# Kernel tuning notes

Hardware: AMD Instinct MI355X
Metric: run time of the kernel (lower is better)

The kernel has to match this reference:

```python
import jax, jax.numpy as jnp
import numpy as np

DIM = 128
HEADS = 8
HEAD_DIM = DIM // HEADS
K = 5          # kernel_size per spatial axis
DIL = 1        # dilation
EPS = 1e-5


def setup_inputs() -> dict:
    key = jax.random.key(0)
    ks = jax.random.split(key, 12)
    s = 0.02
    inp = {
        "x": jax.random.normal(ks[0], (1, DIM, 16, 16, 4), jnp.float32),
        "skip": jax.random.normal(ks[1], (1, DIM, 32, 32, 8), jnp.float32),
        "Wq": jax.random.normal(ks[2], (DIM, DIM), jnp.float32) * s,
        "bq": jnp.zeros((DIM,), jnp.float32),
        "Wk": jax.random.normal(ks[3], (DIM, DIM), jnp.float32) * s,
        "bk": jnp.zeros((DIM,), jnp.float32),
        "Wv": jax.random.normal(ks[4], (DIM, DIM), jnp.float32) * s,
        "bv": jnp.zeros((DIM,), jnp.float32),
        "rpb": jax.random.normal(ks[5], (HEADS, 2 * K - 1, 2 * K - 1, 2 * K - 1), jnp.float32) * s,
        "Wo": jax.random.normal(ks[6], (DIM, DIM), jnp.float32) * s,
        "bo": jnp.zeros((DIM,), jnp.float32),
    }
    return inp


def _instance_norm(t):
    # InstanceNorm3d, affine=False: normalize over spatial dims per (B, C)
    mu = jnp.mean(t, axis=(2, 3, 4), keepdims=True)
    var = jnp.var(t, axis=(2, 3, 4), keepdims=True)
    return (t - mu) * jax.lax.rsqrt(var + EPS)


def _nbr_idx(L):
    # NATTEN-style clamped window: start shifted to stay in bounds
    i = np.arange(L)
    start = np.clip(i - (K // 2) * DIL, 0, L - 1 - (K - 1) * DIL)
    idx = start[:, None] + np.arange(K)[None, :] * DIL  # (L, K)
    rel = (idx - i[:, None]) // DIL + (K - 1)           # (L, K) in [0, 2K-2]
    return jnp.asarray(idx), jnp.asarray(rel)


def reference(x, skip, Wq, bq, Wk, bk, Wv, bv, rpb, Wo, bo):
    x = _instance_norm(x)
    skip = _instance_norm(skip)

    xu = jnp.repeat(jnp.repeat(jnp.repeat(x, 2, axis=2), 2, axis=3), 2, axis=4)

    B, C, H, W, Z = skip.shape
    N = H * W * Z
    xt = xu.transpose(0, 2, 3, 4, 1).reshape(B, N, C)    # queries from upsampled x
    st = skip.transpose(0, 2, 3, 4, 1).reshape(B, N, C)  # keys/values from skip

    def heads(t):
        return t.reshape(B, N, HEADS, HEAD_DIM).transpose(0, 2, 1, 3)  # (B,h,N,d)

    q = heads(xt @ Wq + bq) * (HEAD_DIM ** -0.5)
    k = heads(st @ Wk + bk)
    v = heads(st @ Wv + bv)

    idxH, relH = _nbr_idx(H)
    idxW, relW = _nbr_idx(W)
    idxZ, relZ = _nbr_idx(Z)

    # flattened neighbor token indices: (N, K^3)
    nbr = (idxH[:, None, None, :, None, None] * (W * Z)
           + idxW[None, :, None, None, :, None] * Z
           + idxZ[None, None, :, None, None, :])
    nbr = jnp.broadcast_to(nbr, (H, W, Z, K, K, K)).reshape(N, K ** 3)

    # relative position bias gather: (heads, N, K^3)
    rH = jnp.broadcast_to(relH[:, None, None, :, None, None], (H, W, Z, K, K, K)).reshape(N, K ** 3)
    rW = jnp.broadcast_to(relW[None, :, None, None, :, None], (H, W, Z, K, K, K)).reshape(N, K ** 3)
    rZ = jnp.broadcast_to(relZ[None, None, :, None, None, :], (H, W, Z, K, K, K)).reshape(N, K ** 3)
    bias = rpb[:, rH, rW, rZ]  # (heads, N, K^3)

    kg = jnp.take(k, nbr, axis=2)  # (B, h, N, K^3, d)
    vg = jnp.take(v, nbr, axis=2)

    logits = jnp.einsum('bhnd,bhnkd->bhnk', q, kg) + bias[None]
    attn = jax.nn.softmax(logits, axis=-1)
    out = jnp.einsum('bhnk,bhnkd->bhnd', attn, vg)

    out = out.transpose(0, 2, 1, 3).reshape(B, N, C) @ Wo + bo
    return out.reshape(B, H, W, Z, C).transpose(0, 4, 1, 2, 3)
```

## Files before the change

kernel.cpp:

```cpp
#include <hip/hip_runtime.h>
#include <math.h>

#define DIM 128
#define HEADS 8
#define HD 16
#define NPOS 8192
#define EPS 1e-5f

typedef _Float16 half2_t __attribute__((ext_vector_type(2)));

static __device__ __forceinline__ half2_t u2h(unsigned u) {
    half2_t r; __builtin_memcpy(&r, &u, 4); return r;
}
static __device__ __forceinline__ unsigned pkh(float a, float b) {
    half2_t h; h.x = (_Float16)a; h.y = (_Float16)b;
    unsigned u; __builtin_memcpy(&u, &h, 4); return u;
}
static __device__ __forceinline__ float dot2(unsigned k, unsigned q, float acc) {
#if __has_builtin(__builtin_amdgcn_fdot2)
    return __builtin_amdgcn_fdot2(u2h(k), u2h(q), acc, false);
#else
    half2_t kh = u2h(k), qh = u2h(q);
    acc = fmaf((float)kh.x, (float)qh.x, acc);
    return fmaf((float)kh.y, (float)qh.y, acc);
#endif
}

__global__ __launch_bounds__(256) void stats_kernel(const float* __restrict__ x,
                                                    const float* __restrict__ skip,
                                                    float* __restrict__ ws) {
    int c = blockIdx.x;
    const float* src; int n; float* mu_out; float* rs_out; int ci;
    if (c < DIM) { ci = c; src = x + c * 1024; n = 1024; mu_out = ws; rs_out = ws + DIM; }
    else { ci = c - DIM; src = skip + (size_t)ci * NPOS; n = NPOS; mu_out = ws + 2*DIM; rs_out = ws + 3*DIM; }
    int t = threadIdx.x;
    const float4* s4 = (const float4*)src;
    int n4 = n >> 2;
    float s = 0.f, s2 = 0.f;
    for (int i = t; i < n4; i += 256) {
        float4 v = s4[i];
        s += (v.x + v.y) + (v.z + v.w);
        s2 = fmaf(v.x, v.x, fmaf(v.y, v.y, fmaf(v.z, v.z, fmaf(v.w, v.w, s2))));
    }
    #pragma unroll
    for (int off = 32; off > 0; off >>= 1) {
        s  += __shfl_down(s,  off, 64);
        s2 += __shfl_down(s2, off, 64);
    }
    __shared__ float ls[4], ls2[4];
    int wv = t >> 6;
    if ((t & 63) == 0) { ls[wv] = s; ls2[wv] = s2; }
    __syncthreads();
    if (t == 0) {
        float S  = ls[0] + ls[1] + ls[2] + ls[3];
        float S2 = ls2[0] + ls2[1] + ls2[2] + ls2[3];
        float inv_n = 1.f / (float)n;
        float mu  = S * inv_n;
        float var = S2 * inv_n - mu * mu;
        mu_out[ci] = mu;
        rs_out[ci] = rsqrtf(var + EPS);
    }
}

__global__ __launch_bounds__(256) void qkv_kernel(const float* __restrict__ x,
                                                  const float* __restrict__ skip,
                                                  const float* __restrict__ Wq, const float* __restrict__ bq,
                                                  const float* __restrict__ Wk, const float* __restrict__ bk,
                                                  const float* __restrict__ Wv, const float* __restrict__ bv,
                                                  const float* __restrict__ ws,
                                                  unsigned* __restrict__ q_out,
                                                  unsigned* __restrict__ k_out,
                                                  unsigned* __restrict__ v_out) {
    __shared__ float at[128 * 68];
    __shared__ float wl[128 * 64];
    int which = blockIdx.y;
    if (which == 0 && blockIdx.x >= 16) return;
    int t = threadIdx.x;
    int half  = blockIdx.z;
    int n0 = blockIdx.x * 64;

    const float* W = (which == 0) ? Wq : (which == 1) ? Wk : Wv;
    const float* b = (which == 0) ? bq : (which == 1) ? bk : bv;
    {
        const float4* W4 = (const float4*)W;
        float4* wl4 = (float4*)wl;
        for (int i4 = t; i4 < 2048; i4 += 256) {
            int ci = i4 >> 4, j4 = i4 & 15;
            wl4[ci * 16 + j4] = W4[ci * 32 + half * 16 + j4];
        }
    }
    const float* mu = (which == 0) ? ws : ws + 2*DIM;
    const float* rs = (which == 0) ? ws + DIM : ws + 3*DIM;
    if (which == 0) {
        for (int i4 = t; i4 < 2048; i4 += 256) {
            int ci = i4 >> 4, ln4 = (i4 & 15) * 4;
            float4 f = *(const float4*)(x + ci * 1024 + n0 + ln4);
            float m_ = mu[ci], r_ = rs[ci];
            *(float4*)(at + ci * 68 + ln4) =
                make_float4((f.x - m_) * r_, (f.y - m_) * r_, (f.z - m_) * r_, (f.w - m_) * r_);
        }
    } else {
        for (int i4 = t; i4 < 2048; i4 += 256) {
            int ci = i4 >> 4, ln4 = (i4 & 15) * 4;
            float4 f = *(const float4*)(skip + (size_t)ci * NPOS + n0 + ln4);
            float m_ = mu[ci], r_ = rs[ci];
            *(float4*)(at + ci * 68 + ln4) =
                make_float4((f.x - m_) * r_, (f.y - m_) * r_, (f.z - m_) * r_, (f.w - m_) * r_);
        }
    }
    __syncthreads();

    int pg = t & 15, cg = t >> 4;
    float4 bv4 = *(const float4*)(b + half * 64 + cg * 4);
    float4 acc[4];
    #pragma unroll
    for (int ps = 0; ps < 4; ++ps) acc[ps] = bv4;

    const float* ap = at + pg * 4;
    const float* wp = wl + cg * 4;
    #pragma unroll 4
    for (int ci = 0; ci < 128; ++ci) {
        float4 a4 = *(const float4*)(ap + ci * 68);
        float4 w4 = *(const float4*)(wp + ci * 64);
        float av[4] = { a4.x, a4.y, a4.z, a4.w };
        #pragma unroll
        for (int ps = 0; ps < 4; ++ps) {
            float a = av[ps];
            acc[ps].x = fmaf(a, w4.x, acc[ps].x);
            acc[ps].y = fmaf(a, w4.y, acc[ps].y);
            acc[ps].z = fmaf(a, w4.z, acc[ps].z);
            acc[ps].w = fmaf(a, w4.w, acc[ps].w);
        }
    }
    int p0 = n0 + pg * 4;
    if (which == 0) {
        #pragma unroll
        for (int ps = 0; ps < 4; ++ps) {
            uint2 pk;
            pk.x = pkh(acc[ps].x * 0.25f, acc[ps].y * 0.25f);
            pk.y = pkh(acc[ps].z * 0.25f, acc[ps].w * 0.25f);
            *(uint2*)(q_out + (size_t)(p0 + ps) * 64 + half * 32 + cg * 2) = pk;
        }
    } else {
        unsigned* outp = (which == 1) ? k_out : v_out;
        #pragma unroll
        for (int ps = 0; ps < 4; ++ps) {
            uint2 pk;
            pk.x = pkh(acc[ps].x, acc[ps].y);
            pk.y = pkh(acc[ps].z, acc[ps].w);
            *(uint2*)(outp + (size_t)(p0 + ps) * 64 + half * 32 + cg * 2) = pk;
        }
    }
}

__global__ __launch_bounds__(512, 4) void attn_kernel(const unsigned* __restrict__ qb,
                                                      const unsigned* __restrict__ kb,
                                                      const unsigned* __restrict__ vb,
                                                      const float* __restrict__ rpb,
                                                      float* __restrict__ ao_t) {
    __shared__ uint4 kbf[2 * 544];
    __shared__ uint4 vbf[2 * 544];
    __shared__ float bias_l[744];

    int blk = blockIdx.x;
    int h    = blk & 7;
    int tile = blk >> 3;
    int h0 = (tile >> 3) * 4;
    int w0 = (tile & 7) * 4;
    int bh0 = min(max(h0 - 2, 0), 24);
    int bw0 = min(max(w0 - 2, 0), 24);
    int t = threadIdx.x;

    for (int idx = t; idx < 1024; idx += 512) {
        int c2 = idx & 1;
        int r  = idx >> 1;
        int gz = r & 7;
        int q2 = r >> 3;
        int gh = q2 >> 3, gw = q2 & 7;
        int n = (bh0 + gh) * 256 + (bw0 + gw) * 8 + gz;
        int base = gh * 68 + gw * 8 + ((gz + gw) & 7);
        kbf[c2 * 544 + base] = *(const uint4*)(kb + (size_t)n * 64 + h * 8 + c2 * 4);
        vbf[c2 * 544 + base] = *(const uint4*)(vb + (size_t)n * 64 + h * 8 + c2 * 4);
    }
    for (int idx = t; idx < 744; idx += 512) bias_l[idx] = (idx < 729) ? rpb[h * 729 + idx] : 0.f;
    __syncthreads();

    int s = t & 7, p = t >> 3;
    int ph = p >> 4, pw = (p >> 2) & 3, pzp = p & 3;
    int hc = h0 + ph, wc = w0 + pw, zc0 = pzp * 2;
    int sh = min(max(hc - 2, 0), 27);
    int sw = min(max(wc - 2, 0), 27);
    int sz0 = min(max(zc0 - 2, 0), 3);
    int sz1 = min(max(zc0 - 1, 0), 3);
    int dlt = sz1 - sz0;
    int hb = sh - bh0, wb = sw - bw0;
    int b0 = (sh - hc + 4) * 81 + (sw - wc + 4) * 9 + (sz0 - zc0 + 4);
    int n0pos = hc * 256 + wc * 8 + zc0;

    int qrow = (hc >> 1) * 64 + (wc >> 1) * 4 + pzp;
    uint4 qa = *(const uint4*)(qb + (size_t)qrow * 64 + h * 8);
    uint4 qc = *(const uint4*)(qb + (size_t)qrow * 64 + h * 8 + 4);

    float o0[16], o1[16];
    #pragma unroll
    for (int d = 0; d < 16; ++d) { o0[d] = 0.f; o1[d] = 0.f; }
    float l0 = 0.f, l1 = 0.f;

    int cnt   = 18 + (s < 6);
    int start = s * 18 + min(s, 6);
    int i0 = p & 15;

    for (int it = 0; it < cnt; ++it) {
        int ii = i0 + it; if (ii >= cnt) ii -= cnt;
        int j = start + ii;
        int jh = (j * 2185) >> 16;
        int jr = j - jh * 30;
        int jw = (jr * 43) >> 8;
        int jz = jr - jw * 6;
        int gw = wb + jw;
        int gz = sz0 + jz;
        int base = (hb + jh) * 68 + gw * 8 + ((gz + gw) & 7);
        int joff = jh * 81 + jw * 9 + jz;
        float bias1 = bias_l[b0 + joff - 1];
        float bias0 = bias_l[b0 + joff];

        uint4 ka = kbf[base];
        uint4 k2 = kbf[544 + base];
        float d0 = dot2(ka.x, qa.x, 0.f);
        float d1 = dot2(ka.y, qa.y, 0.f);
        d0 = dot2(ka.z, qa.z, d0);
        d1 = dot2(ka.w, qa.w, d1);
        d0 = dot2(k2.x, qc.x, d0);
        d1 = dot2(k2.y, qc.y, d1);
        d0 = dot2(k2.z, qc.z, d0);
        d1 = dot2(k2.w, qc.w, d1);
        float d = d0 + d1;

        bool v0ok = (jz < 5);
        bool v1ok = ((unsigned)(jz - dlt) < 5u);
        float e0 = __expf(d + bias0);
        float e1 = __expf(d + bias1);
        float pp0 = v0ok ? e0 : 0.f;
        float pp1 = v1ok ? e1 : 0.f;
        l0 += pp0; l1 += pp1;

        uint4 va = vbf[base];
        uint4 v2 = vbf[544 + base];
        #define PV(u, dd) { half2_t vh = u2h(u); float f0 = (float)vh.x, f1 = (float)vh.y; \
            o0[dd]   = fmaf(pp0, f0, o0[dd]);   o1[dd]   = fmaf(pp1, f0, o1[dd]); \
            o0[dd+1] = fmaf(pp0, f1, o0[dd+1]); o1[dd+1] = fmaf(pp1, f1, o1[dd+1]); }
        PV(va.x, 0)  PV(va.y, 2)  PV(va.z, 4)  PV(va.w, 6)
        PV(v2.x, 8)  PV(v2.y, 10) PV(v2.z, 12) PV(v2.w, 14)
        #undef PV
    }

    #pragma unroll
    for (int step = 1; step <= 4; step <<= 1) {
        l0 += __shfl_xor(l0, step, 64);
        l1 += __shfl_xor(l1, step, 64);
        #pragma unroll
        for (int d = 0; d < 16; ++d) {
            o0[d] += __shfl_xor(o0[d], step, 64);
            o1[d] += __shfl_xor(o1[d], step, 64);
        }
    }
    float inv0 = 1.f / l0, inv1 = 1.f / l1;
    int row = h * 16 + 2 * s;
    float2 r0 = make_float2(o0[2*s]     * inv0, o1[2*s]     * inv1);
    float2 r1 = make_float2(o0[2*s + 1] * inv0, o1[2*s + 1] * inv1);
    *(float2*)(ao_t + (size_t)row       * NPOS + n0pos) = r0;
    *(float2*)(ao_t + (size_t)(row + 1) * NPOS + n0pos) = r1;
}

__global__ __launch_bounds__(256) void proj_kernel(const float* __restrict__ ao_t,
                                                   const float* __restrict__ Wo,
                                                   const float* __restrict__ bo,
                                                   float* __restrict__ out) {
    __shared__ float at[128 * 68];
    __shared__ float wl[128 * 64];
    int t = threadIdx.x;
    int half = blockIdx.y;
    int n0 = blockIdx.x * 64;

    {
        const float4* W4 = (const float4*)Wo;
        float4* wl4 = (float4*)wl;
        for (int i4 = t; i4 < 2048; i4 += 256) {
            int ci = i4 >> 4, j4 = i4 & 15;
            wl4[ci * 16 + j4] = W4[ci * 32 + half * 16 + j4];
        }
    }
    for (int i4 = t; i4 < 2048; i4 += 256) {
        int ci = i4 >> 4, ln4 = (i4 & 15) * 4;
        float4 f = *(const float4*)(ao_t + (size_t)ci * NPOS + n0 + ln4);
        *(float4*)(at + ci * 68 + ln4) = f;
    }
    __syncthreads();

    int pg = t & 15, cg = t >> 4;
    float4 bv4 = *(const float4*)(bo + half * 64 + cg * 4);
    float4 acc[4];
    #pragma unroll
    for (int ps = 0; ps < 4; ++ps) acc[ps] = bv4;

    const float* ap = at + pg * 4;
    const float* wp = wl + cg * 4;
    #pragma unroll 4
    for (int ci = 0; ci < 128; ++ci) {
        float4 a4 = *(const float4*)(ap + ci * 68);
        float4 w4 = *(const float4*)(wp + ci * 64);
        float av[4] = { a4.x, a4.y, a4.z, a4.w };
        #pragma unroll
        for (int ps = 0; ps < 4; ++ps) {
            float a = av[ps];
            acc[ps].x = fmaf(a, w4.x, acc[ps].x);
            acc[ps].y = fmaf(a, w4.y, acc[ps].y);
            acc[ps].z = fmaf(a, w4.z, acc[ps].z);
            acc[ps].w = fmaf(a, w4.w, acc[ps].w);
        }
    }
    int p0 = n0 + pg * 4;
    int jbase = half * 64 + cg * 4;
    *(float4*)(out + (size_t)(jbase + 0) * NPOS + p0) = make_float4(acc[0].x, acc[1].x, acc[2].x, acc[3].x);
    *(float4*)(out + (size_t)(jbase + 1) * NPOS + p0) = make_float4(acc[0].y, acc[1].y, acc[2].y, acc[3].y);
    *(float4*)(out + (size_t)(jbase + 2) * NPOS + p0) = make_float4(acc[0].z, acc[1].z, acc[2].z, acc[3].z);
    *(float4*)(out + (size_t)(jbase + 3) * NPOS + p0) = make_float4(acc[0].w, acc[1].w, acc[2].w, acc[3].w);
}

extern "C" void kernel_launch(void* const* d_in, const int* in_sizes, int n_in,
                              void* d_out, int out_size, void* d_ws, size_t ws_size,
                              hipStream_t stream) {
    const float* x    = (const float*)d_in[0];
    const float* skip = (const float*)d_in[1];
    const float* Wq   = (const float*)d_in[2];
    const float* bq   = (const float*)d_in[3];
    const float* Wk   = (const float*)d_in[4];
    const float* bk   = (const float*)d_in[5];
    const float* Wv   = (const float*)d_in[6];
    const float* bv   = (const float*)d_in[7];
    const float* rpb  = (const float*)d_in[8];
    const float* Wo   = (const float*)d_in[9];
    const float* bo   = (const float*)d_in[10];
    float* out = (float*)d_out;

    float*    ws   = (float*)d_ws;
    unsigned* q    = (unsigned*)(ws + 512);
    unsigned* kbp  = q + 1024 * 64;
    unsigned* vbp  = kbp + (size_t)NPOS * 64;
    float*    ao_t = (float*)(vbp + (size_t)NPOS * 64);

    stats_kernel<<<256, 256, 0, stream>>>(x, skip, ws);
    qkv_kernel<<<dim3(128, 3, 2), 256, 0, stream>>>(x, skip, Wq, bq, Wk, bk, Wv, bv, ws, q, kbp, vbp);
    attn_kernel<<<512, 512, 0, stream>>>(q, kbp, vbp, rpb, ao_t);
    proj_kernel<<<dim3(128, 2), 256, 0, stream>>>(ao_t, Wo, bo, out);
}
```

Before: 129.7 us.

## Use 128x128 fp16-staged tiles with 8x8 register blocking in QKV and projection GEMMs

Both the QKV and output-projection kernels now handle 128 positions by all 128 output channels per block. Activations and weights are staged in shared memory as fp16 to fit the larger tile, and each thread accumulates an 8x8 register block instead of 4x4. This removes the split over output-channel halves, so inputs are loaded once and each shared-memory read feeds more FMAs. In exchange the grids shrink to 64 blocks (fewer than the CU count), register pressure rises, and the projection input ao_t is now rounded to fp16, which adds precision loss.

```diff
diff --git a/kernel.cpp b/kernel.cpp
--- a/kernel.cpp
+++ b/kernel.cpp
@@ -71,84 +71,98 @@
                                                   unsigned* __restrict__ q_out,
                                                   unsigned* __restrict__ k_out,
                                                   unsigned* __restrict__ v_out) {
-    __shared__ float at[128 * 68];
-    __shared__ float wl[128 * 64];
+    __shared__ __align__(16) _Float16 ah[128 * 128];
+    __shared__ __align__(16) _Float16 wh[128 * 128];
     int which = blockIdx.y;
-    if (which == 0 && blockIdx.x >= 16) return;
+    if (which == 0 && blockIdx.x >= 8) return;
     int t = threadIdx.x;
-    int half  = blockIdx.z;
-    int n0 = blockIdx.x * 64;
+    int n0 = blockIdx.x * 128;
 
     const float* W = (which == 0) ? Wq : (which == 1) ? Wk : Wv;
     const float* b = (which == 0) ? bq : (which == 1) ? bk : bv;
+    const float* mu = (which == 0) ? ws : ws + 2*DIM;
+    const float* rs = (which == 0) ? ws + DIM : ws + 3*DIM;
+
     {
         const float4* W4 = (const float4*)W;
-        float4* wl4 = (float4*)wl;
-        for (int i4 = t; i4 < 2048; i4 += 256) {
-            int ci = i4 >> 4, j4 = i4 & 15;
-            wl4[ci * 16 + j4] = W4[ci * 32 + half * 16 + j4];
-        }
-    }
-    const float* mu = (which == 0) ? ws : ws + 2*DIM;
-    const float* rs = (which == 0) ? ws + DIM : ws + 3*DIM;
+        for (int i4 = t; i4 < 4096; i4 += 256) {
+            int ci = i4 >> 5, j4 = i4 & 31;
+            float4 w = W4[ci * 32 + j4];
+            *(uint2*)&wh[ci * 128 + j4 * 4] = make_uint2(pkh(w.x, w.y), pkh(w.z, w.w));
+        }
+    }
     if (which == 0) {
-        for (int i4 = t; i4 < 2048; i4 += 256) {
-            int ci = i4 >> 4, ln4 = (i4 & 15) * 4;
-            float4 f = *(const float4*)(x + ci * 1024 + n0 + ln4);
+        const float4* x4 = (const float4*)x;
+        for (int i4 = t; i4 < 4096; i4 += 256) {
+            int ci = i4 >> 5, j4 = i4 & 31;
+            float4 f = x4[ci * 256 + (n0 >> 2) + j4];
             float m_ = mu[ci], r_ = rs[ci];
-            *(float4*)(at + ci * 68 + ln4) =
-                make_float4((f.x - m_) * r_, (f.y - m_) * r_, (f.z - m_) * r_, (f.w - m_) * r_);
+            *(uint2*)&ah[ci * 128 + j4 * 4] =
+                make_uint2(pkh((f.x - m_) * r_, (f.y - m_) * r_),
+                           pkh((f.z - m_) * r_, (f.w - m_) * r_));
         }
     } else {
-        for (int i4 = t; i4 < 2048; i4 += 256) {
-            int ci = i4 >> 4, ln4 = (i4 & 15) * 4;
-            float4 f = *(const float4*)(skip + (size_t)ci * NPOS + n0 + ln4);
+        for (int i4 = t; i4 < 4096; i4 += 256) {
+            int ci = i4 >> 5, j4 = i4 & 31;
+            float4 f = *(const float4*)(skip + (size_t)ci * NPOS + n0 + j4 * 4);
             float m_ = mu[ci], r_ = rs[ci];
-            *(float4*)(at + ci * 68 + ln4) =
-                make_float4((f.x - m_) * r_, (f.y - m_) * r_, (f.z - m_) * r_, (f.w - m_) * r_);
+            *(uint2*)&ah[ci * 128 + j4 * 4] =
+                make_uint2(pkh((f.x - m_) * r_, (f.y - m_) * r_),
+                           pkh((f.z - m_) * r_, (f.w - m_) * r_));
         }
     }
     __syncthreads();
 
     int pg = t & 15, cg = t >> 4;
-    float4 bv4 = *(const float4*)(b + half * 64 + cg * 4);
-    float4 acc[4];
-    #pragma unroll
-    for (int ps = 0; ps < 4; ++ps) acc[ps] = bv4;
-
-    const float* ap = at + pg * 4;
-    const float* wp = wl + cg * 4;
+    float4 b0 = *(const float4*)(b + cg * 8);
+    float4 b1 = *(const float4*)(b + cg * 8 + 4);
+    float acc[8][8];
+    #pragma unroll
+    for (int p = 0; p < 8; ++p) {
+        acc[p][0] = b0.x; acc[p][1] = b0.y; acc[p][2] = b0.z; acc[p][3] = b0.w;
+        acc[p][4] = b1.x; acc[p][5] = b1.y; acc[p][6] = b1.z; acc[p][7] = b1.w;
+    }
+
+    const _Float16* ap = ah + pg * 8;
+    const _Float16* wp = wh + cg * 8;
     #pragma unroll 4
     for (int ci = 0; ci < 128; ++ci) {
-        float4 a4 = *(const float4*)(ap + ci * 68);
-        float4 w4 = *(const float4*)(wp + ci * 64);
-        float av[4] = { a4.x, a4.y, a4.z, a4.w };
-        #pragma unroll
-        for (int ps = 0; ps < 4; ++ps) {
-            float a = av[ps];
-            acc[ps].x = fmaf(a, w4.x, acc[ps].x);
-            acc[ps].y = fmaf(a, w4.y, acc[ps].y);
-            acc[ps].z = fmaf(a, w4.z, acc[ps].z);
-            acc[ps].w = fmaf(a, w4.w, acc[ps].w);
-        }
-    }
-    int p0 = n0 + pg * 4;
+        uint4 au = *(const uint4*)(ap + ci * 128);
+        uint4 wu = *(const uint4*)(wp + ci * 128);
+        half2_t a0 = u2h(au.x), a1 = u2h(au.y), a2 = u2h(au.z), a3 = u2h(au.w);
+        half2_t w0 = u2h(wu.x), w1 = u2h(wu.y), w2 = u2h(wu.z), w3 = u2h(wu.w);
+        float af[8] = { (float)a0.x, (float)a0.y, (float)a1.x, (float)a1.y,
+                        (float)a2.x, (float)a2.y, (float)a3.x, (float)a3.y };
+        float wf[8] = { (float)w0.x, (float)w0.y, (float)w1.x, (float)w1.y,
+                        (float)w2.x, (float)w2.y, (float)w3.x, (float)w3.y };
+        #pragma unroll
+        for (int p = 0; p < 8; ++p)
+            #pragma unroll
+            for (int c = 0; c < 8; ++c)
+                acc[p][c] = fmaf(af[p], wf[c], acc[p][c]);
+    }
+
+    int p0 = n0 + pg * 8;
     if (which == 0) {
         #pragma unroll
-        for (int ps = 0; ps < 4; ++ps) {
-            uint2 pk;
-            pk.x = pkh(acc[ps].x * 0.25f, acc[ps].y * 0.25f);
-            pk.y = pkh(acc[ps].z * 0.25f, acc[ps].w * 0.25f);
-            *(uint2*)(q_out + (size_t)(p0 + ps) * 64 + half * 32 + cg * 2) = pk;
+        for (int p = 0; p < 8; ++p) {
+            uint4 o;
+            o.x = pkh(acc[p][0] * 0.25f, acc[p][1] * 0.25f);
+            o.y = pkh(acc[p][2] * 0.25f, acc[p][3] * 0.25f);
+            o.z = pkh(acc[p][4] * 0.25f, acc[p][5] * 0.25f);
+            o.w = pkh(acc[p][6] * 0.25f, acc[p][7] * 0.25f);
+            *(uint4*)(q_out + (size_t)(p0 + p) * 64 + cg * 4) = o;
         }
     } else {
         unsigned* outp = (which == 1) ? k_out : v_out;
         #pragma unroll
-        for (int ps = 0; ps < 4; ++ps) {
-            uint2 pk;
-            pk.x = pkh(acc[ps].x, acc[ps].y);
-            pk.y = pkh(acc[ps].z, acc[ps].w);
-            *(uint2*)(outp + (size_t)(p0 + ps) * 64 + half * 32 + cg * 2) = pk;
+        for (int p = 0; p < 8; ++p) {
+            uint4 o;
+            o.x = pkh(acc[p][0], acc[p][1]);
+            o.y = pkh(acc[p][2], acc[p][3]);
+            o.z = pkh(acc[p][4], acc[p][5]);
+            o.w = pkh(acc[p][6], acc[p][7]);
+            *(uint4*)(outp + (size_t)(p0 + p) * 64 + cg * 4) = o;
         }
     }
 }
@@ -276,55 +290,63 @@
                                                    const float* __restrict__ Wo,
                                                    const float* __restrict__ bo,
                                                    float* __restrict__ out) {
-    __shared__ float at[128 * 68];
-    __shared__ float wl[128 * 64];
+    __shared__ __align__(16) _Float16 ah[128 * 128];
+    __shared__ __align__(16) _Float16 wh[128 * 128];
     int t = threadIdx.x;
-    int half = blockIdx.y;
-    int n0 = blockIdx.x * 64;
+    int n0 = blockIdx.x * 128;
 
     {
         const float4* W4 = (const float4*)Wo;
-        float4* wl4 = (float4*)wl;
-        for (int i4 = t; i4 < 2048; i4 += 256) {
-            int ci = i4 >> 4, j4 = i4 & 15;
-            wl4[ci * 16 + j4] = W4[ci * 32 + half * 16 + j4];
-        }
-    }
-    for (int i4 = t; i4 < 2048; i4 += 256) {
-        int ci = i4 >> 4, ln4 = (i4 & 15) * 4;
-        float4 f = *(const float4*)(ao_t + (size_t)ci * NPOS + n0 + ln4);
-        *(float4*)(at + ci * 68 + ln4) = f;
+        for (int i4 = t; i4 < 4096; i4 += 256) {
+            int ci = i4 >> 5, j4 = i4 & 31;
+            float4 w = W4[ci * 32 + j4];
+            *(uint2*)&wh[ci * 128 + j4 * 4] = make_uint2(pkh(w.x, w.y), pkh(w.z, w.w));
+        }
+    }
+    for (int i4 = t; i4 < 4096; i4 += 256) {
+        int ci = i4 >> 5, j4 = i4 & 31;
+        float4 f = *(const float4*)(ao_t + (size_t)ci * NPOS + n0 + j4 * 4);
+        *(uint2*)&ah[ci * 128 + j4 * 4] = make_uint2(pkh(f.x, f.y), pkh(f.z, f.w));
     }
     __syncthreads();
 
     int pg = t & 15, cg = t >> 4;
-    float4 bv4 = *(const float4*)(bo + half * 64 + cg * 4);
-    float4 acc[4];
-    #pragma unroll
-    for (int ps = 0; ps < 4; ++ps) acc[ps] = bv4;
-
-    const float* ap = at + pg * 4;
-    const float* wp = wl + cg * 4;
+    float4 b0 = *(const float4*)(bo + cg * 8);
+    float4 b1 = *(const float4*)(bo + cg * 8 + 4);
+    float acc[8][8];
+    #pragma unroll
+    for (int p = 0; p < 8; ++p) {
+        acc[p][0] = b0.x; acc[p][1] = b0.y; acc[p][2] = b0.z; acc[p][3] = b0.w;
+        acc[p][4] = b1.x; acc[p][5] = b1.y; acc[p][6] = b1.z; acc[p][7] = b1.w;
+    }
+
+    const _Float16* ap = ah + pg * 8;
+    const _Float16* wp = wh + cg * 8;
     #pragma unroll 4
     for (int ci = 0; ci < 128; ++ci) {
-        float4 a4 = *(const float4*)(ap + ci * 68);
-        float4 w4 = *(const float4*)(wp + ci * 64);
-        float av[4] = { a4.x, a4.y, a4.z, a4.w };
-        #pragma unroll
-        for (int ps = 0; ps < 4; ++ps) {
-            float a = av[ps];
-            acc[ps].x = fmaf(a, w4.x, acc[ps].x);
-            acc[ps].y = fmaf(a, w4.y, acc[ps].y);
-            acc[ps].z = fmaf(a, w4.z, acc[ps].z);
-            acc[ps].w = fmaf(a, w4.w, acc[ps].w);
-        }
-    }
-    int p0 = n0 + pg * 4;
-    int jbase = half * 64 + cg * 4;
-    *(float4*)(out + (size_t)(jbase + 0) * NPOS + p0) = make_float4(acc[0].x, acc[1].x, acc[2].x, acc[3].x);
-    *(float4*)(out + (size_t)(jbase + 1) * NPOS + p0) = make_float4(acc[0].y, acc[1].y, acc[2].y, acc[3].y);
-    *(float4*)(out + (size_t)(jbase + 2) * NPOS + p0) = make_float4(acc[0].z, acc[1].z, acc[2].z, acc[3].z);
-    *(float4*)(out + (size_t)(jbase + 3) * NPOS + p0) = make_float4(acc[0].w, acc[1].w, acc[2].w, acc[3].w);
+        uint4 au = *(const uint4*)(ap + ci * 128);
+        uint4 wu = *(const uint4*)(wp + ci * 128);
+        half2_t a0 = u2h(au.x), a1 = u2h(au.y), a2 = u2h(au.z), a3 = u2h(au.w);
+        half2_t w0 = u2h(wu.x), w1 = u2h(wu.y), w2 = u2h(wu.z), w3 = u2h(wu.w);
+        float af[8] = { (float)a0.x, (float)a0.y, (float)a1.x, (float)a1.y,
+                        (float)a2.x, (float)a2.y, (float)a3.x, (float)a3.y };
+        float wf[8] = { (float)w0.x, (float)w0.y, (float)w1.x, (float)w1.y,
+                        (float)w2.x, (float)w2.y, (float)w3.x, (float)w3.y };
+        #pragma unroll
+        for (int p = 0; p < 8; ++p)
+            #pragma unroll
+            for (int c = 0; c < 8; ++c)
+                acc[p][c] = fmaf(af[p], wf[c], acc[p][c]);
+    }
+
+    int p0 = n0 + pg * 8;
+    int co0 = cg * 8;
+    #pragma unroll
+    for (int c = 0; c < 8; ++c) {
+        float* op = out + (size_t)(co0 + c) * NPOS + p0;
+        *(float4*)op       = make_float4(acc[0][c], acc[1][c], acc[2][c], acc[3][c]);
+        *(float4*)(op + 4) = make_float4(acc[4][c], acc[5][c], acc[6][c], acc[7][c]);
+    }
 }
 
 extern "C" void kernel_launch(void* const* d_in, const int* in_sizes, int n_in,
@@ -350,7 +372,7 @@
     float*    ao_t = (float*)(vbp + (size_t)NPOS * 64);
 
     stats_kernel<<<256, 256, 0, stream>>>(x, skip, ws);
-    qkv_kernel<<<dim3(128, 3, 2), 256, 0, stream>>>(x, skip, Wq, bq, Wk, bk, Wv, bv, ws, q, kbp, vbp);
+    qkv_kernel<<<dim3(64, 3), 256, 0, stream>>>(x, skip, Wq, bq, Wk, bk, Wv, bv, ws, q, kbp, vbp);
     attn_kernel<<<512, 512, 0, stream>>>(q, kbp, vbp, rpb, ao_t);
-    proj_kernel<<<dim3(128, 2), 256, 0, stream>>>(ao_t, Wo, bo, out);
-}
+    proj_kernel<<<64, 256, 0, stream>>>(ao_t, Wo, bo, out);
+}
```

Result: slower. 153.4 us (+18.3%).

## Replace fp32 QKV and output projections with fp16 MFMA GEMM kernel

Applied to the files above, without the earlier changes.

Converts the four weight matrices to transposed fp16 inside the stats kernel. Replaces the scalar-FMA QKV and output projection kernels with one unified MFMA 16x16x32 GEMM kernel that keeps weight fragments in registers and stages activations in swizzled LDS. This removes the fp32 FMA cost and the LDS weight staging. In exchange it adds fp16 rounding of activations and weights (including ao and Wo in the output projection), and uses strided per-element global loads for the A tile.

```diff
diff --git a/kernel.cpp b/kernel.cpp
--- a/kernel.cpp
+++ b/kernel.cpp
@@ -8,6 +8,8 @@
 #define EPS 1e-5f
 
 typedef _Float16 half2_t __attribute__((ext_vector_type(2)));
+typedef _Float16 f16x8  __attribute__((ext_vector_type(8)));
+typedef float    f32x4  __attribute__((ext_vector_type(4)));
 
 static __device__ __forceinline__ half2_t u2h(unsigned u) {
     half2_t r; __builtin_memcpy(&r, &u, 4); return r;
@@ -28,12 +30,35 @@
 
 __global__ __launch_bounds__(256) void stats_kernel(const float* __restrict__ x,
                                                     const float* __restrict__ skip,
-                                                    float* __restrict__ ws) {
+                                                    const float* __restrict__ Wq,
+                                                    const float* __restrict__ Wk,
+                                                    const float* __restrict__ Wv,
+                                                    const float* __restrict__ Wo,
+                                                    float* __restrict__ ws,
+                                                    unsigned short* __restrict__ Wt) {
     int c = blockIdx.x;
+    int t = threadIdx.x;
+    if (c >= 256) {
+        int c2 = c - 256;
+        int m = c2 >> 2, chunk = c2 & 3;
+        const float* Wsrc = (m == 0) ? Wq : (m == 1) ? Wk : (m == 2) ? Wv : Wo;
+        unsigned short* dst = Wt + (size_t)m * 16384;
+        int co = t & 127, half = t >> 7;
+        int ci0 = chunk * 32 + half * 16;
+        unsigned pk8[8];
+        #pragma unroll
+        for (int j = 0; j < 8; ++j) {
+            float a = Wsrc[(ci0 + 2*j    ) * 128 + co];
+            float b = Wsrc[(ci0 + 2*j + 1) * 128 + co];
+            pk8[j] = pkh(a, b);
+        }
+        *(uint4*)(dst + (size_t)co * 128 + ci0)     = *(uint4*)&pk8[0];
+        *(uint4*)(dst + (size_t)co * 128 + ci0 + 8) = *(uint4*)&pk8[4];
+        return;
+    }
     const float* src; int n; float* mu_out; float* rs_out; int ci;
     if (c < DIM) { ci = c; src = x + c * 1024; n = 1024; mu_out = ws; rs_out = ws + DIM; }
     else { ci = c - DIM; src = skip + (size_t)ci * NPOS; n = NPOS; mu_out = ws + 2*DIM; rs_out = ws + 3*DIM; }
-    int t = threadIdx.x;
     const float4* s4 = (const float4*)src;
     int n4 = n >> 2;
     float s = 0.f, s2 = 0.f;
@@ -62,93 +87,117 @@
     }
 }
 
-__global__ __launch_bounds__(256) void qkv_kernel(const float* __restrict__ x,
-                                                  const float* __restrict__ skip,
-                                                  const float* __restrict__ Wq, const float* __restrict__ bq,
-                                                  const float* __restrict__ Wk, const float* __restrict__ bk,
-                                                  const float* __restrict__ Wv, const float* __restrict__ bv,
-                                                  const float* __restrict__ ws,
-                                                  unsigned* __restrict__ q_out,
-                                                  unsigned* __restrict__ k_out,
-                                                  unsigned* __restrict__ v_out) {
-    __shared__ float at[128 * 68];
-    __shared__ float wl[128 * 64];
-    int which = blockIdx.y;
-    if (which == 0 && blockIdx.x >= 16) return;
+__global__ __launch_bounds__(256) void gemm_kernel(int phase,
+    const float* __restrict__ x, const float* __restrict__ skip,
+    const float* __restrict__ ao_t,
+    const unsigned short* __restrict__ Wt_all,
+    const float* __restrict__ bq, const float* __restrict__ bk,
+    const float* __restrict__ bv, const float* __restrict__ bo,
+    const float* __restrict__ ws,
+    unsigned* __restrict__ q_out, unsigned* __restrict__ k_out,
+    unsigned* __restrict__ v_out, float* __restrict__ out) {
+    __shared__ __align__(16) unsigned short A_lds[32 * 128];
+    int bx = blockIdx.x;
+    const float* A; int lda; const float* mu; const float* rs;
+    const unsigned short* Wt; const float* bias; float scale = 1.f;
+    unsigned* opk = nullptr; float* of = nullptr; int n0;
+    if (phase == 0) {
+        if (bx < 256)      { A = skip; lda = NPOS; mu = ws + 256; rs = ws + 384;
+                             Wt = Wt_all + 16384;     bias = bk; opk = k_out; n0 = bx * 32; }
+        else if (bx < 512) { A = skip; lda = NPOS; mu = ws + 256; rs = ws + 384;
+                             Wt = Wt_all + 2 * 16384; bias = bv; opk = v_out; n0 = (bx - 256) * 32; }
+        else               { A = x;    lda = 1024; mu = ws;       rs = ws + 128;
+                             Wt = Wt_all;             bias = bq; opk = q_out; n0 = (bx - 512) * 32;
+                             scale = 0.25f; }
+    } else {
+        A = ao_t; lda = NPOS; mu = nullptr; rs = nullptr;
+        Wt = Wt_all + 3 * 16384; bias = bo; of = out; n0 = bx * 32;
+    }
     int t = threadIdx.x;
-    int half  = blockIdx.z;
-    int n0 = blockIdx.x * 64;
-
-    const float* W = (which == 0) ? Wq : (which == 1) ? Wk : Wv;
-    const float* b = (which == 0) ? bq : (which == 1) ? bk : bv;
+    int lane = t & 63, w = t >> 6;
+
+    int co_f = w * 32 + (lane & 15);
+    int kf   = (lane >> 4) * 8;
+    uint4 wf[2][4];
+    #pragma unroll
+    for (int mt = 0; mt < 2; ++mt)
+        #pragma unroll
+        for (int k4 = 0; k4 < 4; ++k4)
+            wf[mt][k4] = *(const uint4*)(Wt + (size_t)(co_f + mt * 16) * 128 + k4 * 32 + kf);
+
     {
-        const float4* W4 = (const float4*)W;
-        float4* wl4 = (float4*)wl;
-        for (int i4 = t; i4 < 2048; i4 += 256) {
-            int ci = i4 >> 4, j4 = i4 & 15;
-            wl4[ci * 16 + j4] = W4[ci * 32 + half * 16 + j4];
-        }
-    }
-    const float* mu = (which == 0) ? ws : ws + 2*DIM;
-    const float* rs = (which == 0) ? ws + DIM : ws + 3*DIM;
-    if (which == 0) {
-        for (int i4 = t; i4 < 2048; i4 += 256) {
-            int ci = i4 >> 4, ln4 = (i4 & 15) * 4;
-            float4 f = *(const float4*)(x + ci * 1024 + n0 + ln4);
-            float m_ = mu[ci], r_ = rs[ci];
-            *(float4*)(at + ci * 68 + ln4) =
-                make_float4((f.x - m_) * r_, (f.y - m_) * r_, (f.z - m_) * r_, (f.w - m_) * r_);
-        }
-    } else {
-        for (int i4 = t; i4 < 2048; i4 += 256) {
-            int ci = i4 >> 4, ln4 = (i4 & 15) * 4;
-            float4 f = *(const float4*)(skip + (size_t)ci * NPOS + n0 + ln4);
-            float m_ = mu[ci], r_ = rs[ci];
-            *(float4*)(at + ci * 68 + ln4) =
-                make_float4((f.x - m_) * r_, (f.y - m_) * r_, (f.z - m_) * r_, (f.w - m_) * r_);
+        int pos = t & 31, g = t >> 5;
+        const float* ap = A + n0 + pos;
+        float f[16];
+        #pragma unroll
+        for (int rep = 0; rep < 4; ++rep) {
+            int ci0 = g * 4 + rep * 32;
+            f[rep*4+0] = ap[(size_t)(ci0    ) * lda];
+            f[rep*4+1] = ap[(size_t)(ci0 + 1) * lda];
+            f[rep*4+2] = ap[(size_t)(ci0 + 2) * lda];
+            f[rep*4+3] = ap[(size_t)(ci0 + 3) * lda];
+        }
+        #pragma unroll
+        for (int rep = 0; rep < 4; ++rep) {
+            int ci0 = g * 4 + rep * 32;
+            float f0 = f[rep*4+0], f1 = f[rep*4+1], f2 = f[rep*4+2], f3 = f[rep*4+3];
+            if (phase == 0) {
+                f0 = (f0 - mu[ci0    ]) * rs[ci0    ];
+                f1 = (f1 - mu[ci0 + 1]) * rs[ci0 + 1];
+                f2 = (f2 - mu[ci0 + 2]) * rs[ci0 + 2];
+                f3 = (f3 - mu[ci0 + 3]) * rs[ci0 + 3];
+            }
+            int byte = (pos * 256 + ci0 * 2) ^ ((pos & 7) << 4);
+            *(uint2*)((char*)A_lds + byte) = make_uint2(pkh(f0, f1), pkh(f2, f3));
         }
     }
     __syncthreads();
 
-    int pg = t & 15, cg = t >> 4;
-    float4 bv4 = *(const float4*)(b + half * 64 + cg * 4);
-    float4 acc[4];
-    #pragma unroll
-    for (int ps = 0; ps < 4; ++ps) acc[ps] = bv4;
-
-    const float* ap = at + pg * 4;
-    const float* wp = wl + cg * 4;
-    #pragma unroll 4
-    for (int ci = 0; ci < 128; ++ci) {
-        float4 a4 = *(const float4*)(ap + ci * 68);
-        float4 w4 = *(const float4*)(wp + ci * 64);
-        float av[4] = { a4.x, a4.y, a4.z, a4.w };
-        #pragma unroll
-        for (int ps = 0; ps < 4; ++ps) {
-            float a = av[ps];
-            acc[ps].x = fmaf(a, w4.x, acc[ps].x);
-            acc[ps].y = fmaf(a, w4.y, acc[ps].y);
-            acc[ps].z = fmaf(a, w4.z, acc[ps].z);
-            acc[ps].w = fmaf(a, w4.w, acc[ps].w);
-        }
-    }
-    int p0 = n0 + pg * 4;
-    if (which == 0) {
-        #pragma unroll
-        for (int ps = 0; ps < 4; ++ps) {
-            uint2 pk;
-            pk.x = pkh(acc[ps].x * 0.25f, acc[ps].y * 0.25f);
-            pk.y = pkh(acc[ps].z * 0.25f, acc[ps].w * 0.25f);
-            *(uint2*)(q_out + (size_t)(p0 + ps) * 64 + half * 32 + cg * 2) = pk;
-        }
-    } else {
-        unsigned* outp = (which == 1) ? k_out : v_out;
-        #pragma unroll
-        for (int ps = 0; ps < 4; ++ps) {
-            uint2 pk;
-            pk.x = pkh(acc[ps].x, acc[ps].y);
-            pk.y = pkh(acc[ps].z, acc[ps].w);
-            *(uint2*)(outp + (size_t)(p0 + ps) * 64 + half * 32 + cg * 2) = pk;
+    f32x4 acc[2][2];
+    #pragma unroll
+    for (int mt = 0; mt < 2; ++mt)
+        #pragma unroll
+        for (int nt = 0; nt < 2; ++nt)
+            acc[mt][nt] = (f32x4){0.f, 0.f, 0.f, 0.f};
+    #pragma unroll
+    for (int k4 = 0; k4 < 4; ++k4) {
+        f16x8 af[2];
+        #pragma unroll
+        for (int nt = 0; nt < 2; ++nt) {
+            int pos = nt * 16 + (lane & 15);
+            int byte = (pos * 256 + (k4 * 32 + kf) * 2) ^ ((pos & 7) << 4);
+            uint4 u = *(const uint4*)((const char*)A_lds + byte);
+            __builtin_memcpy(&af[nt], &u, 16);
+        }
+        #pragma unroll
+        for (int mt = 0; mt < 2; ++mt) {
+            f16x8 wfr; __builtin_memcpy(&wfr, &wf[mt][k4], 16);
+            acc[mt][0] = __builtin_amdgcn_mfma_f32_16x16x32_f16(wfr, af[0], acc[mt][0], 0, 0, 0);
+            acc[mt][1] = __builtin_amdgcn_mfma_f32_16x16x32_f16(wfr, af[1], acc[mt][1], 0, 0, 0);
+        }
+    }
+
+    int colp  = lane & 15;
+    int rquad = (lane >> 4) * 4;
+    #pragma unroll
+    for (int mt = 0; mt < 2; ++mt) {
+        int co = w * 32 + mt * 16 + rquad;
+        float4 bv4 = *(const float4*)(bias + co);
+        #pragma unroll
+        for (int nt = 0; nt < 2; ++nt) {
+            int pos = n0 + nt * 16 + colp;
+            float v0 = (acc[mt][nt][0] + bv4.x) * scale;
+            float v1 = (acc[mt][nt][1] + bv4.y) * scale;
+            float v2 = (acc[mt][nt][2] + bv4.z) * scale;
+            float v3 = (acc[mt][nt][3] + bv4.w) * scale;
+            if (phase == 0) {
+                *(uint2*)(opk + (size_t)pos * 64 + (co >> 1)) = make_uint2(pkh(v0, v1), pkh(v2, v3));
+            } else {
+                of[(size_t)(co    ) * NPOS + pos] = v0;
+                of[(size_t)(co + 1) * NPOS + pos] = v1;
+                of[(size_t)(co + 2) * NPOS + pos] = v2;
+                of[(size_t)(co + 3) * NPOS + pos] = v3;
+            }
         }
     }
 }
@@ -270,61 +319,6 @@
     float2 r1 = make_float2(o0[2*s + 1] * inv0, o1[2*s + 1] * inv1);
     *(float2*)(ao_t + (size_t)row       * NPOS + n0pos) = r0;
     *(float2*)(ao_t + (size_t)(row + 1) * NPOS + n0pos) = r1;
-}
-
-__global__ __launch_bounds__(256) void proj_kernel(const float* __restrict__ ao_t,
-                                                   const float* __restrict__ Wo,
-                                                   const float* __restrict__ bo,
-                                                   float* __restrict__ out) {
-    __shared__ float at[128 * 68];
-    __shared__ float wl[128 * 64];
-    int t = threadIdx.x;
-    int half = blockIdx.y;
-    int n0 = blockIdx.x * 64;
-
-    {
-        const float4* W4 = (const float4*)Wo;
-        float4* wl4 = (float4*)wl;
-        for (int i4 = t; i4 < 2048; i4 += 256) {
-            int ci = i4 >> 4, j4 = i4 & 15;
-            wl4[ci * 16 + j4] = W4[ci * 32 + half * 16 + j4];
-        }
-    }
-    for (int i4 = t; i4 < 2048; i4 += 256) {
-        int ci = i4 >> 4, ln4 = (i4 & 15) * 4;
-        float4 f = *(const float4*)(ao_t + (size_t)ci * NPOS + n0 + ln4);
-        *(float4*)(at + ci * 68 + ln4) = f;
-    }
-    __syncthreads();
-
-    int pg = t & 15, cg = t >> 4;
-    float4 bv4 = *(const float4*)(bo + half * 64 + cg * 4);
-    float4 acc[4];
-    #pragma unroll
-    for (int ps = 0; ps < 4; ++ps) acc[ps] = bv4;
-
-    const float* ap = at + pg * 4;
-    const float* wp = wl + cg * 4;
-    #pragma unroll 4
-    for (int ci = 0; ci < 128; ++ci) {
-        float4 a4 = *(const float4*)(ap + ci * 68);
-        float4 w4 = *(const float4*)(wp + ci * 64);
-        float av[4] = { a4.x, a4.y, a4.z, a4.w };
-        #pragma unroll
-        for (int ps = 0; ps < 4; ++ps) {
-            float a = av[ps];
-            acc[ps].x = fmaf(a, w4.x, acc[ps].x);
-            acc[ps].y = fmaf(a, w4.y, acc[ps].y);
-            acc[ps].z = fmaf(a, w4.z, acc[ps].z);
-            acc[ps].w = fmaf(a, w4.w, acc[ps].w);
-        }
-    }
-    int p0 = n0 + pg * 4;
-    int jbase = half * 64 + cg * 4;
-    *(float4*)(out + (size_t)(jbase + 0) * NPOS + p0) = make_float4(acc[0].x, acc[1].x, acc[2].x, acc[3].x);
-    *(float4*)(out + (size_t)(jbase + 1) * NPOS + p0) = make_float4(acc[0].y, acc[1].y, acc[2].y, acc[3].y);
-    *(float4*)(out + (size_t)(jbase + 2) * NPOS + p0) = make_float4(acc[0].z, acc[1].z, acc[2].z, acc[3].z);
-    *(float4*)(out + (size_t)(jbase + 3) * NPOS + p0) = make_float4(acc[0].w, acc[1].w, acc[2].w, acc[3].w);
 }
 
 extern "C" void kernel_launch(void* const* d_in, const int* in_sizes, int n_in,
@@ -343,14 +337,17 @@
     const float* bo   = (const float*)d_in[10];
     float* out = (float*)d_out;
 
-    float*    ws   = (float*)d_ws;
-    unsigned* q    = (unsigned*)(ws + 512);
-    unsigned* kbp  = q + 1024 * 64;
-    unsigned* vbp  = kbp + (size_t)NPOS * 64;
+    float*          ws  = (float*)d_ws;
+    unsigned short* Wt  = (unsigned short*)(ws + 512);
+    unsigned* q   = (unsigned*)(Wt + 4 * 16384);
+    unsigned* kbp = q + 1024 * 64;
+    unsigned* vbp = kbp + (size_t)NPOS * 64;
     float*    ao_t = (float*)(vbp + (size_t)NPOS * 64);
 
-    stats_kernel<<<256, 256, 0, stream>>>(x, skip, ws);
-    qkv_kernel<<<dim3(128, 3, 2), 256, 0, stream>>>(x, skip, Wq, bq, Wk, bk, Wv, bv, ws, q, kbp, vbp);
+    stats_kernel<<<272, 256, 0, stream>>>(x, skip, Wq, Wk, Wv, Wo, ws, Wt);
+    gemm_kernel<<<544, 256, 0, stream>>>(0, x, skip, ao_t, Wt, bq, bk, bv, bo, ws,
+                                         q, kbp, vbp, out);
     attn_kernel<<<512, 512, 0, stream>>>(q, kbp, vbp, rpb, ao_t);
-    proj_kernel<<<dim3(128, 2), 256, 0, stream>>>(ao_t, Wo, bo, out);
-}
+    gemm_kernel<<<256, 256, 0, stream>>>(1, x, skip, ao_t, Wt, bq, bk, bv, bo, ws,
+                                         q, kbp, vbp, out);
+}
```

After: 115.7 us. 10.8% less time.
